# Optimization experiments

Hardware: AMD Instinct MI355X
Metric: run time of the kernel (lower is better)

The kernel has to match this reference:

```python
import jax, jax.numpy as jnp
import numpy as np

B, CIN, H, W = 32, 64, 128, 128
HID, OUT, E, S, R = 64, 64, 8, 2, 16
TOP_K = 2
TEMP = 2.0
BN_EPS = 1e-5


def setup_inputs() -> dict:
    key = jax.random.key(0)
    ks = jax.random.split(key, 16)
    sc = lambda fan: 1.0 / np.sqrt(fan)
    h2 = 2 * HID
    return {
        "x": jax.random.normal(ks[0], (B, CIN, H, W), jnp.float32),
        "fe_w": jax.random.normal(ks[1], (HID, CIN), jnp.float32) * sc(CIN),
        "fe_b": jnp.zeros((HID,), jnp.float32),
        "s_w": jax.random.normal(ks[2], (S, OUT, HID), jnp.float32) * sc(HID),
        "s_b": jnp.zeros((S, OUT), jnp.float32),
        "e_w": jax.random.normal(ks[3], (E, OUT, HID), jnp.float32) * sc(HID),
        "e_b": jnp.zeros((E, OUT), jnp.float32),
        "g1_w": jax.random.normal(ks[4], (h2, HID), jnp.float32) * sc(HID),
        "g1_b": jnp.zeros((h2,), jnp.float32),
        "bn1_g": jnp.ones((h2,), jnp.float32),
        "bn1_b": jnp.zeros((h2,), jnp.float32),
        "ca1_w": jax.random.normal(ks[5], (h2 // R, h2), jnp.float32) * sc(h2),
        "ca1_b": jnp.zeros((h2 // R,), jnp.float32),
        "ca2_w": jax.random.normal(ks[6], (h2, h2 // R), jnp.float32) * sc(h2 // R),
        "ca2_b": jnp.zeros((h2,), jnp.float32),
        "g2_w": jax.random.normal(ks[7], (HID, h2), jnp.float32) * sc(h2),
        "g2_b": jnp.zeros((HID,), jnp.float32),
        "bn2_g": jnp.ones((HID,), jnp.float32),
        "bn2_b": jnp.zeros((HID,), jnp.float32),
        "g3_w": jax.random.normal(ks[8], (E, HID), jnp.float32) * sc(HID),
        "g3_b": jnp.zeros((E,), jnp.float32),
    }


def _gelu(v):
    return jax.nn.gelu(v, approximate=False)


def _bn_eval(v, g, b):
    # BatchNorm eval mode with running_mean=0, running_var=1
    return v * (g / np.sqrt(1.0 + BN_EPS)) + b


def reference(x, fe_w, fe_b, s_w, s_b, e_w, e_b, g1_w, g1_b, bn1_g, bn1_b,
              ca1_w, ca1_b, ca2_w, ca2_b, g2_w, g2_b, bn2_g, bn2_b, g3_w, g3_b):
    # feature extractor: 1x1 conv + GELU
    features = _gelu(jnp.einsum('bchw,oc->bohw', x, fe_w) + fe_b[None, :, None, None])

    # shared experts: mean of S expert outputs (sum / S)
    shared = _gelu(jnp.einsum('bchw,soc->bsohw', features, s_w)
                   + s_b[None, :, :, None, None]).mean(axis=1)

    # gating on globally pooled features [B, HID]
    gf = features.mean(axis=(2, 3))
    h1 = _gelu(_bn_eval(gf @ g1_w.T + g1_b, bn1_g, bn1_b))  # [B, 2*HID]
    # ChannelAttention on 1x1 spatial: avg_pool == max_pool == identity
    att = _gelu(h1 @ ca1_w.T + ca1_b) @ ca2_w.T + ca2_b
    h1 = h1 * jax.nn.sigmoid(att + att)  # avg_out + max_out are identical
    hh = _gelu(_bn_eval(h1 @ g2_w.T + g2_b, bn2_g, bn2_b))  # [B, HID]
    scores = hh @ g3_w.T + g3_b  # [B, E]

    top_vals, top_idx = jax.lax.top_k(scores, TOP_K)
    top_w = jax.nn.softmax(top_vals / TEMP, axis=1)  # [B, TOP_K]
    # dense per-(sample, expert) weights
    dense_w = jnp.zeros((x.shape[0], E), scores.dtype).at[
        jnp.arange(x.shape[0])[:, None], top_idx].add(top_w)

    # all experts on full batch, then weighted accumulate (matches original loop)
    eo = _gelu(jnp.einsum('bchw,eoc->beohw', features, e_w)
               + e_b[None, :, :, None, None])  # [B, E, OUT, H, W]
    routed = jnp.einsum('beohw,be->bohw', eo, dense_w)

    return shared + routed
```

## Files before the change

### kernel.cpp

```cpp
#include <hip/hip_runtime.h>
#include <hip/hip_bf16.h>
#include <stdint.h>

#define HW 16384

typedef __bf16 bf16_t;
typedef bf16_t bf16x8 __attribute__((ext_vector_type(8)));
typedef float f32x4 __attribute__((ext_vector_type(4)));

__device__ __forceinline__ float gelu_f(float x) {
    float t = x * fmaf(x * x, 0.044715f, 1.0f);
    float e = __builtin_amdgcn_exp2f(-2.3022083f * t);
    return x * __builtin_amdgcn_rcpf(1.0f + e);
}

__device__ __forceinline__ uint32_t pk2(float a, float b) {
    union { bf16_t h[2]; uint32_t u; } z;
    z.h[0] = (bf16_t)a; z.h[1] = (bf16_t)b;
    return z.u;
}

__device__ __forceinline__ void load16_to_lds(const float* g, float* lds) {
    __builtin_amdgcn_global_load_lds(
        (const __attribute__((address_space(1))) uint32_t*)g,
        (__attribute__((address_space(3))) uint32_t*)lds, 16, 0, 0);
}

__device__ __forceinline__ bf16x8 frag8(const float* src) {
    float4 lo = ((const float4*)src)[0];
    float4 hi = ((const float4*)src)[1];
    bf16x8 r;
    r[0] = (bf16_t)lo.x; r[1] = (bf16_t)lo.y; r[2] = (bf16_t)lo.z; r[3] = (bf16_t)lo.w;
    r[4] = (bf16_t)hi.x; r[5] = (bf16_t)hi.y; r[6] = (bf16_t)hi.z; r[7] = (bf16_t)hi.w;
    return r;
}

__device__ __forceinline__ bf16x8 frag44(const float* a, const float* b) {
    float4 lo = *(const float4*)a;
    float4 hi = *(const float4*)b;
    bf16x8 r;
    r[0] = (bf16_t)lo.x; r[1] = (bf16_t)lo.y; r[2] = (bf16_t)lo.z; r[3] = (bf16_t)lo.w;
    r[4] = (bf16_t)hi.x; r[5] = (bf16_t)hi.y; r[6] = (bf16_t)hi.z; r[7] = (bf16_t)hi.w;
    return r;
}

#define PIN asm volatile("" ::: "memory")

__global__ __launch_bounds__(256, 2)
void k1_feat(const float* __restrict__ x, const float* __restrict__ fe_w,
             const float* __restrict__ fe_b, bf16_t* __restrict__ feat,
             float* __restrict__ gf_part) {
    __shared__ float xs[4][2][32 * 64];
    __shared__ float gf4[4][64];

    int tid = threadIdx.x;
    int lane = tid & 63;
    int wid = tid >> 6;
    int r16 = lane & 15;
    int g = lane >> 4;
    int gtile0 = blockIdx.x * 16 + wid * 4;
    int b = gtile0 >> 9;
    int px0 = (gtile0 & 511) * 32;

    bf16x8 A[4][2];
    f32x4 bias[4];
#pragma unroll
    for (int ot = 0; ot < 4; ++ot) {
#pragma unroll
        for (int kh = 0; kh < 2; ++kh)
            A[ot][kh] = frag8(fe_w + (ot * 16 + r16) * 64 + kh * 32 + g * 8);
        bias[ot] = *(const f32x4*)(fe_b + ot * 16 + g * 4);
    }
    PIN;

    float* xw = &xs[wid][0][0];
    int rl = lane >> 3;
    int ch0 = lane & 7;

    auto STAGE = [&](int buf, int t) {
#pragma unroll
        for (int s = 0; s < 8; ++s) {
            int row = s * 8 + rl;
            int gch = ch0 ^ ((s & 3) << 1);
            const float* gsrc = x + (size_t)(b * 64 + row) * HW + px0 + t * 32 + gch * 4;
            load16_to_lds(gsrc, xw + buf * 2048 + s * 256);
        }
    };

    int cm0 = ((((r16 >> 2) + 0) ^ (g << 1)) << 2) + (r16 & 3);
    int cm1 = ((((r16 >> 2) + 4) ^ (g << 1)) << 2) + (r16 & 3);

    float gfp[4][4] = {};
    bf16_t* featb = feat + (size_t)b * HW * 64;

    auto COMPUTE = [&](int buf, int t) {
        const float* xb = xw + buf * 2048;
        bf16x8 B00, B10, B01, B11;
#pragma unroll
        for (int j = 0; j < 8; ++j) {
            int ro0 = (g * 8 + j) * 32;
            int ro1 = (32 + g * 8 + j) * 32;
            B00[j] = (bf16_t)xb[ro0 + cm0];
            B10[j] = (bf16_t)xb[ro0 + cm1];
            B01[j] = (bf16_t)xb[ro1 + cm0];
            B11[j] = (bf16_t)xb[ro1 + cm1];
        }
        f32x4 y0[4], y1[4];
#pragma unroll
        for (int ot = 0; ot < 4; ++ot) {
            f32x4 z = {0.f, 0.f, 0.f, 0.f};
            z = __builtin_amdgcn_mfma_f32_16x16x32_bf16(A[ot][0], B00, z, 0, 0, 0);
            y0[ot] = __builtin_amdgcn_mfma_f32_16x16x32_bf16(A[ot][1], B01, z, 0, 0, 0);
            f32x4 w = {0.f, 0.f, 0.f, 0.f};
            w = __builtin_amdgcn_mfma_f32_16x16x32_bf16(A[ot][0], B10, w, 0, 0, 0);
            y1[ot] = __builtin_amdgcn_mfma_f32_16x16x32_bf16(A[ot][1], B11, w, 0, 0, 0);
        }
#pragma unroll
        for (int a = 0; a < 2; ++a) {
            f32x4* y = a ? y1 : y0;
            float vals[4][4];
#pragma unroll
            for (int ot = 0; ot < 4; ++ot)
#pragma unroll
                for (int r = 0; r < 4; ++r) {
                    float v = gelu_f(y[ot][r] + bias[ot][r]);
                    gfp[ot][r] += v;
                    vals[ot][r] = v;
                }
            uint4 lo, hi;
            lo.x = pk2(vals[0][0], vals[0][1]); lo.y = pk2(vals[0][2], vals[0][3]);
            lo.z = pk2(vals[1][0], vals[1][1]); lo.w = pk2(vals[1][2], vals[1][3]);
            hi.x = pk2(vals[2][0], vals[2][1]); hi.y = pk2(vals[2][2], vals[2][3]);
            hi.z = pk2(vals[3][0], vals[3][1]); hi.w = pk2(vals[3][2], vals[3][3]);
            int px = px0 + t * 32 + a * 16 + r16;
            uint4* dst = (uint4*)(featb + (size_t)px * 64 + g * 16);
            dst[0] = lo;
            dst[1] = hi;
        }
    };

    STAGE(0, 0);
    STAGE(1, 1);
    PIN;
    asm volatile("s_waitcnt vmcnt(8)" ::: "memory");
    COMPUTE(0, 0);
    PIN;
    STAGE(0, 2);
    PIN;
    asm volatile("s_waitcnt vmcnt(12)" ::: "memory");
    COMPUTE(1, 1);
    PIN;
    STAGE(1, 3);
    PIN;
    asm volatile("s_waitcnt vmcnt(12)" ::: "memory");
    COMPUTE(0, 2);
    PIN;
    asm volatile("s_waitcnt vmcnt(4)" ::: "memory");
    COMPUTE(1, 3);

#pragma unroll
    for (int ot = 0; ot < 4; ++ot)
#pragma unroll
        for (int r = 0; r < 4; ++r) {
            float v = gfp[ot][r];
            v += __shfl_xor(v, 1);
            v += __shfl_xor(v, 2);
            v += __shfl_xor(v, 4);
            v += __shfl_xor(v, 8);
            if (r16 == 0) gf4[wid][ot * 16 + g * 4 + r] = v;
        }
    __syncthreads();
    if (tid < 64)
        gf_part[(size_t)blockIdx.x * 64 + tid] =
            gf4[0][tid] + gf4[1][tid] + gf4[2][tid] + gf4[3][tid];
}

__global__ __launch_bounds__(256)
void k2_gate(const float* __restrict__ gf_part,
             const float* __restrict__ g1_w, const float* __restrict__ g1_b,
             const float* __restrict__ bn1_g, const float* __restrict__ bn1_b,
             const float* __restrict__ ca1_w, const float* __restrict__ ca1_b,
             const float* __restrict__ ca2_w, const float* __restrict__ ca2_b,
             const float* __restrict__ g2_w, const float* __restrict__ g2_b,
             const float* __restrict__ bn2_g, const float* __restrict__ bn2_b,
             const float* __restrict__ g3_w, const float* __restrict__ g3_b,
             int* __restrict__ gidx, float* __restrict__ gw) {
    __shared__ float w1t[128 * 65];
    __shared__ float wc1[8 * 129];
    __shared__ float wc2[128 * 9];
    __shared__ float w2t[64 * 129];
    __shared__ float w3[8 * 65];
    __shared__ float gf[64], h1[128], a1[8], hh[64], sc[8];
    const float R1 = 0.99999500003749969f;
    int tid = threadIdx.x;
    int b = blockIdx.x;

    for (int i = tid; i < 2048; i += 256) {
        float4 v = ((const float4*)g1_w)[i];
        float* d = w1t + (i >> 4) * 65 + (i & 15) * 4;
        d[0] = v.x; d[1] = v.y; d[2] = v.z; d[3] = v.w;
    }
    for (int i = tid; i < 2048; i += 256) {
        float4 v = ((const float4*)g2_w)[i];
        float* d = w2t + (i >> 5) * 129 + (i & 31) * 4;
        d[0] = v.x; d[1] = v.y; d[2] = v.z; d[3] = v.w;
    }
    if (tid < 256) {
        int i = tid;
        float4 v = ((const float4*)ca1_w)[i];
        float* d = wc1 + (i >> 5) * 129 + (i & 31) * 4;
        d[0] = v.x; d[1] = v.y; d[2] = v.z; d[3] = v.w;
    }
    if (tid < 256) {
        int i = tid;
        float4 v = ((const float4*)ca2_w)[i];
        float* d = wc2 + (i >> 1) * 9 + (i & 1) * 4;
        d[0] = v.x; d[1] = v.y; d[2] = v.z; d[3] = v.w;
    }
    if (tid < 128) {
        int i = tid;
        float4 v = ((const float4*)g3_w)[i];
        float* d = w3 + (i >> 4) * 65 + (i & 15) * 4;
        d[0] = v.x; d[1] = v.y; d[2] = v.z; d[3] = v.w;
    }
    if (tid < 64) {
        float s0 = 0.f, s1 = 0.f;
        const float* gp = gf_part + (size_t)b * 32 * 64 + tid;
#pragma unroll 8
        for (int i = 0; i < 32; i += 2) {
            s0 += gp[(size_t)(i + 0) * 64];
            s1 += gp[(size_t)(i + 1) * 64];
        }
        gf[tid] = (s0 + s1) * (1.0f / 16384.0f);
    }
    __syncthreads();

    if (tid < 128) {
        int j = tid;
        float s0 = 0.f, s1 = 0.f;
#pragma unroll 8
        for (int c = 0; c < 64; c += 2) {
            s0 += gf[c] * w1t[j * 65 + c];
            s1 += gf[c + 1] * w1t[j * 65 + c + 1];
        }
        float s = g1_b[j] + s0 + s1;
        s = s * (bn1_g[j] * R1) + bn1_b[j];
        h1[j] = gelu_f(s);
    }
    __syncthreads();
    if (tid < 8) {
        int j = tid;
        float s0 = 0.f, s1 = 0.f;
#pragma unroll 8
        for (int c = 0; c < 128; c += 2) {
            s0 += h1[c] * wc1[j * 129 + c];
            s1 += h1[c + 1] * wc1[j * 129 + c + 1];
        }
        a1[j] = gelu_f(ca1_b[j] + s0 + s1);
    }
    __syncthreads();
    if (tid < 128) {
        int j = tid;
        float s = ca2_b[j];
#pragma unroll
        for (int r = 0; r < 8; ++r) s += a1[r] * wc2[j * 9 + r];
        float e2 = __builtin_amdgcn_exp2f(-2.8853901f * s);
        h1[j] = h1[j] * __builtin_amdgcn_rcpf(1.0f + e2);
    }
    __syncthreads();
    if (tid < 64) {
        int j = tid;
        float s0 = 0.f, s1 = 0.f;
#pragma unroll 8
        for (int c = 0; c < 128; c += 2) {
            s0 += h1[c] * w2t[j * 129 + c];
            s1 += h1[c + 1] * w2t[j * 129 + c + 1];
        }
        float s = g2_b[j] + s0 + s1;
        s = s * (bn2_g[j] * R1) + bn2_b[j];
        hh[j] = gelu_f(s);
    }
    __syncthreads();
    if (tid < 8) {
        int j = tid;
        float s0 = 0.f, s1 = 0.f;
#pragma unroll 8
        for (int c = 0; c < 64; c += 2) {
            s0 += hh[c] * w3[j * 65 + c];
            s1 += hh[c + 1] * w3[j * 65 + c + 1];
        }
        sc[j] = g3_b[j] + s0 + s1;
    }
    __syncthreads();
    if (tid == 0) {
        float v0 = -1e30f, v1 = -1e30f;
        int i0 = 0, i1 = 0;
#pragma unroll
        for (int e = 0; e < 8; ++e) {
            float s = sc[e];
            if (s > v0) { v1 = v0; i1 = i0; v0 = s; i0 = e; }
            else if (s > v1) { v1 = s; i1 = e; }
        }
        float t = __builtin_amdgcn_exp2f(0.7213475f * (v1 - v0));
        float den = __builtin_amdgcn_rcpf(1.0f + t);
        gidx[b * 2] = i0; gidx[b * 2 + 1] = i1;
        gw[b * 2] = den; gw[b * 2 + 1] = t * den;
    }
}

__global__ __launch_bounds__(256, 4)
void k3_out(const bf16_t* __restrict__ feat, const float* __restrict__ s_w,
            const float* __restrict__ s_b, const float* __restrict__ e_w,
            const float* __restrict__ e_b, const int* __restrict__ gidx,
            const float* __restrict__ gw, float* __restrict__ out) {
    int tid = threadIdx.x;
    int lane = tid & 63, wid = tid >> 6;
    int r16 = lane & 15, g = lane >> 4;
    int b = blockIdx.x >> 6;
    int stripe = blockIdx.x & 63;

    int i0 = gidx[2 * b], i1 = gidx[2 * b + 1];
    float coef[4] = {0.5f, 0.5f, gw[2 * b], gw[2 * b + 1]};
    const float* Wm[4] = {s_w, s_w + 4096,
                          e_w + (size_t)i0 * 4096, e_w + (size_t)i1 * 4096};
    const float* Bv[4] = {s_b, s_b + 64, e_b + i0 * 64, e_b + i1 * 64};

    bf16x8 Wf[4][2];
    float bias[4];
    int row = wid * 16 + r16;
#pragma unroll
    for (int m = 0; m < 4; ++m) {
#pragma unroll
        for (int kh = 0; kh < 2; ++kh) {
            int base = (g & 1) * 32 + (kh * 2 + (g >> 1)) * 4;
            Wf[m][kh] = frag44(Wm[m] + row * 64 + base,
                               Wm[m] + row * 64 + base + 16);
        }
        bias[m] = Bv[m][row];
    }

    const uint4* fb = (const uint4*)(feat + (size_t)b * HW * 64);
    float* outb = out + ((size_t)b * 64 + row) * HW + stripe * 256;
    int pbase = stripe * 256 + r16;

    auto BODY = [&](int t, uint4 u0, uint4 u1) {
        bf16x8 F0 = __builtin_bit_cast(bf16x8, u0);
        bf16x8 F1 = __builtin_bit_cast(bf16x8, u1);
        f32x4 acc = {0.f, 0.f, 0.f, 0.f};
#pragma unroll
        for (int m = 0; m < 4; ++m) {
            f32x4 y = {0.f, 0.f, 0.f, 0.f};
            y = __builtin_amdgcn_mfma_f32_16x16x32_bf16(F0, Wf[m][0], y, 0, 0, 0);
            y = __builtin_amdgcn_mfma_f32_16x16x32_bf16(F1, Wf[m][1], y, 0, 0, 0);
#pragma unroll
            for (int r = 0; r < 4; ++r)
                acc[r] += coef[m] * gelu_f(y[r] + bias[m]);
        }
        float4 st = {acc[0], acc[1], acc[2], acc[3]};
        *(float4*)(outb + t * 16 + g * 4) = st;
    };

    uint4 a0 = fb[(size_t)pbase * 8 + g];
    uint4 a1 = fb[(size_t)pbase * 8 + 4 + g];
    uint4 b0 = fb[(size_t)(pbase + 16) * 8 + g];
    uint4 b1 = fb[(size_t)(pbase + 16) * 8 + 4 + g];
#pragma unroll
    for (int t = 0; t < 14; t += 2) {
        uint4 n0 = fb[(size_t)(pbase + (t + 2) * 16) * 8 + g];
        uint4 n1 = fb[(size_t)(pbase + (t + 2) * 16) * 8 + 4 + g];
        BODY(t, a0, a1); a0 = n0; a1 = n1;
        uint4 m0 = fb[(size_t)(pbase + (t + 3) * 16) * 8 + g];
        uint4 m1 = fb[(size_t)(pbase + (t + 3) * 16) * 8 + 4 + g];
        BODY(t + 1, b0, b1); b0 = m0; b1 = m1;
    }
    BODY(14, a0, a1);
    BODY(15, b0, b1);
}

extern "C" void kernel_launch(void* const* d_in, const int* in_sizes, int n_in,
                              void* d_out, int out_size, void* d_ws, size_t ws_size,
                              hipStream_t stream) {
    (void)in_sizes; (void)n_in; (void)out_size; (void)ws_size;
    const float* x     = (const float*)d_in[0];
    const float* fe_w  = (const float*)d_in[1];
    const float* fe_b  = (const float*)d_in[2];
    const float* s_w   = (const float*)d_in[3];
    const float* s_b   = (const float*)d_in[4];
    const float* e_w   = (const float*)d_in[5];
    const float* e_b   = (const float*)d_in[6];
    const float* g1_w  = (const float*)d_in[7];
    const float* g1_b  = (const float*)d_in[8];
    const float* bn1_g = (const float*)d_in[9];
    const float* bn1_b = (const float*)d_in[10];
    const float* ca1_w = (const float*)d_in[11];
    const float* ca1_b = (const float*)d_in[12];
    const float* ca2_w = (const float*)d_in[13];
    const float* ca2_b = (const float*)d_in[14];
    const float* g2_w  = (const float*)d_in[15];
    const float* g2_b  = (const float*)d_in[16];
    const float* bn2_g = (const float*)d_in[17];
    const float* bn2_b = (const float*)d_in[18];
    const float* g3_w  = (const float*)d_in[19];
    const float* g3_b  = (const float*)d_in[20];
    float* out = (float*)d_out;

    char* wsb = (char*)d_ws;
    bf16_t* feat   = (bf16_t*)wsb;
    float* gf_part = (float*)(wsb + 67108864);
    int* gidx      = (int*)(wsb + 67108864 + 1048576);
    float* gwts    = (float*)(wsb + 67108864 + 1048576 + 256);

    k1_feat<<<1024, 256, 0, stream>>>(x, fe_w, fe_b, feat, gf_part);
    k2_gate<<<32, 256, 0, stream>>>(gf_part, g1_w, g1_b, bn1_g, bn1_b, ca1_w, ca1_b,
                                    ca2_w, ca2_b, g2_w, g2_b, bn2_g, bn2_b, g3_w, g3_b,
                                    gidx, gwts);
    k3_out<<<2048, 256, 0, stream>>>(feat, s_w, s_b, e_w, e_b, gidx, gwts, out);
}
```

Baseline: 342.2 us.

## Replace LDS double-buffered staging with direct global loads in feature kernel

After: 352.4 us. 1.03x slower.

```diff
diff --git a/kernel.cpp b/kernel.cpp
--- a/kernel.cpp
+++ b/kernel.cpp
@@ -18,12 +18,6 @@
     union { bf16_t h[2]; uint32_t u; } z;
     z.h[0] = (bf16_t)a; z.h[1] = (bf16_t)b;
     return z.u;
-}
-
-__device__ __forceinline__ void load16_to_lds(const float* g, float* lds) {
-    __builtin_amdgcn_global_load_lds(
-        (const __attribute__((address_space(1))) uint32_t*)g,
-        (__attribute__((address_space(3))) uint32_t*)lds, 16, 0, 0);
 }
 
 __device__ __forceinline__ bf16x8 frag8(const float* src) {
@@ -44,13 +38,10 @@
     return r;
 }
 
-#define PIN asm volatile("" ::: "memory")
-
-__global__ __launch_bounds__(256, 2)
+__global__ __launch_bounds__(256, 4)
 void k1_feat(const float* __restrict__ x, const float* __restrict__ fe_w,
              const float* __restrict__ fe_b, bf16_t* __restrict__ feat,
              float* __restrict__ gf_part) {
-    __shared__ float xs[4][2][32 * 64];
     __shared__ float gf4[4][64];
 
     int tid = threadIdx.x;
@@ -71,40 +62,35 @@
             A[ot][kh] = frag8(fe_w + (ot * 16 + r16) * 64 + kh * 32 + g * 8);
         bias[ot] = *(const f32x4*)(fe_b + ot * 16 + g * 4);
     }
-    PIN;
-
-    float* xw = &xs[wid][0][0];
-    int rl = lane >> 3;
-    int ch0 = lane & 7;
-
-    auto STAGE = [&](int buf, int t) {
-#pragma unroll
-        for (int s = 0; s < 8; ++s) {
-            int row = s * 8 + rl;
-            int gch = ch0 ^ ((s & 3) << 1);
-            const float* gsrc = x + (size_t)(b * 64 + row) * HW + px0 + t * 32 + gch * 4;
-            load16_to_lds(gsrc, xw + buf * 2048 + s * 256);
-        }
-    };
-
-    int cm0 = ((((r16 >> 2) + 0) ^ (g << 1)) << 2) + (r16 & 3);
-    int cm1 = ((((r16 >> 2) + 4) ^ (g << 1)) << 2) + (r16 & 3);
+
+    const float* xgl = x + (size_t)(b * 64 + g * 8) * HW;
+    const float* xgh = xgl + (size_t)32 * HW;
 
     float gfp[4][4] = {};
     bf16_t* featb = feat + (size_t)b * HW * 64;
 
-    auto COMPUTE = [&](int buf, int t) {
-        const float* xb = xw + buf * 2048;
+#pragma unroll 1
+    for (int t = 0; t < 4; ++t) {
+        int p = px0 + t * 32 + r16;
+
+        float v00[8], v10[8], v01[8], v11[8];
+#pragma unroll
+        for (int j = 0; j < 8; ++j) {
+            size_t o = (size_t)j * HW + p;
+            v00[j] = xgl[o];
+            v10[j] = xgl[o + 16];
+            v01[j] = xgh[o];
+            v11[j] = xgh[o + 16];
+        }
         bf16x8 B00, B10, B01, B11;
 #pragma unroll
         for (int j = 0; j < 8; ++j) {
-            int ro0 = (g * 8 + j) * 32;
-            int ro1 = (32 + g * 8 + j) * 32;
-            B00[j] = (bf16_t)xb[ro0 + cm0];
-            B10[j] = (bf16_t)xb[ro0 + cm1];
-            B01[j] = (bf16_t)xb[ro1 + cm0];
-            B11[j] = (bf16_t)xb[ro1 + cm1];
-        }
+            B00[j] = (bf16_t)v00[j];
+            B10[j] = (bf16_t)v10[j];
+            B01[j] = (bf16_t)v01[j];
+            B11[j] = (bf16_t)v11[j];
+        }
+
         f32x4 y0[4], y1[4];
 #pragma unroll
         for (int ot = 0; ot < 4; ++ot) {
@@ -115,6 +101,7 @@
             w = __builtin_amdgcn_mfma_f32_16x16x32_bf16(A[ot][0], B10, w, 0, 0, 0);
             y1[ot] = __builtin_amdgcn_mfma_f32_16x16x32_bf16(A[ot][1], B11, w, 0, 0, 0);
         }
+
 #pragma unroll
         for (int a = 0; a < 2; ++a) {
             f32x4* y = a ? y1 : y0;
@@ -137,26 +124,7 @@
             dst[0] = lo;
             dst[1] = hi;
         }
-    };
-
-    STAGE(0, 0);
-    STAGE(1, 1);
-    PIN;
-    asm volatile("s_waitcnt vmcnt(8)" ::: "memory");
-    COMPUTE(0, 0);
-    PIN;
-    STAGE(0, 2);
-    PIN;
-    asm volatile("s_waitcnt vmcnt(12)" ::: "memory");
-    COMPUTE(1, 1);
-    PIN;
-    STAGE(1, 3);
-    PIN;
-    asm volatile("s_waitcnt vmcnt(12)" ::: "memory");
-    COMPUTE(0, 2);
-    PIN;
-    asm volatile("s_waitcnt vmcnt(4)" ::: "memory");
-    COMPUTE(1, 3);
+    }
 
 #pragma unroll
     for (int ot = 0; ot < 4; ++ot)
```
